# Kernel optimization log

Hardware: AMD Instinct MI355X
Metric: run time of the kernel (lower is better)

The kernel has to match this reference:

```python
import jax, jax.numpy as jnp
import numpy as np

T, EQ, N, H, K_HOPS, K_POOL = 4, 4096, 8192, 32, 2, 3


def setup_inputs() -> dict:
    key = jax.random.key(0)
    ks = jax.random.split(key, 6)
    s = 1.0 / np.sqrt(H)
    return {
        "edge_index": jax.random.randint(ks[0], (T, 2, EQ), 0, N),
        "W_gcn": jax.random.normal(ks[1], (1, H), jnp.float32) * 0.5,
        "b_gcn": jnp.zeros((H,), jnp.float32),
        "W_ih": jax.random.normal(ks[2], (3 * H, H), jnp.float32) * s,
        "W_hh": jax.random.normal(ks[3], (3 * H, H), jnp.float32) * s,
        "b_ih": jax.random.normal(ks[4], (3 * H,), jnp.float32) * s,
        "b_hh": jax.random.normal(ks[5], (3 * H,), jnp.float32) * s,
        "num_nodes": N,
    }


def _reach(seeds, src, dst, num_nodes, k):
    # k-hop reachability masks, PyG k_hop_subgraph flow='source_to_target'
    # (walk edges backwards: add sources of edges whose target is reached).
    eq = seeds.shape[0]
    R = jnp.zeros((eq, num_nodes), bool).at[jnp.arange(eq), seeds].set(True)
    for _ in range(k):
        R = R.at[:, src].max(R[:, dst])
    return R


def reference(edge_index, W_gcn, b_gcn, W_ih, W_hh, b_ih, b_hh, num_nodes):
    uq = edge_index[-1, 0]  # [EQ] query-edge sources (last snapshot)
    vq = edge_index[-1, 1]  # [EQ] query-edge targets

    def per_graph(ei):
        src, dst = ei[0], ei[1]
        Ru = _reach(uq, src, dst, num_nodes, K_HOPS)  # [EQ, N]
        Rv = _reach(vq, src, dst, num_nodes, K_HOPS)
        # union of the two k-hop subgraph edge sets (dedup via OR)
        incl = (Ru[:, src] & Ru[:, dst]) | (Rv[:, src] & Rv[:, dst])  # [EQ, Eg]
        # per-node in-degree within the merged subgraph (degree of edge_index[1])
        deg = jnp.zeros((uq.shape[0], num_nodes), jnp.float32)
        deg = deg.at[:, dst].add(incl.astype(jnp.float32))
        # global_sort_pool(k=3): top-3 nodes by the (single) degree feature,
        # zero-padded if the subgraph has <3 positive-degree nodes
        return jax.lax.top_k(deg, K_POOL)[0]  # [EQ, 3]

    tops = jax.vmap(per_graph)(edge_index)  # [T, EQ, 3]

    # GCNConv(1, H) on the 3 pooled nodes (self-loop-normalized: x @ W + b), ReLU
    h = jax.nn.relu(tops[..., None] * W_gcn[0] + b_gcn)  # [T, EQ, 3, H]

    # GRU over T snapshots, batch = EQ*3 pooled nodes
    x_seq = h.reshape(h.shape[0], -1, H)  # [T, EQ*3, H]
    h0 = jnp.zeros((x_seq.shape[1], H), x_seq.dtype)

    def cell(hprev, x):
        gi = x @ W_ih.T + b_ih
        gh = hprev @ W_hh.T + b_hh
        ir, iz, ig = jnp.split(gi, 3, axis=-1)
        hr, hz, hg = jnp.split(gh, 3, axis=-1)
        r = jax.nn.sigmoid(ir + hr)
        z = jax.nn.sigmoid(iz + hz)
        n = jnp.tanh(ig + r * hg)
        hnew = (1.0 - z) * n + z * hprev
        return hnew, None

    hn, _ = jax.lax.scan(cell, h0, x_seq)
    # stacked hidden_list: one [3, H] state per query edge
    return hn.reshape(-1, K_POOL, H)  # [EQ, 3, H]
```

## Files before the change

kernel.cpp:

```cpp
#include <hip/hip_runtime.h>
#include <hip/hip_bf16.h>
#include <math.h>

#define T_SNAP 4
#define EQn 4096
#define Nn 8192
#define Hn 32
#define NWn (Nn/32)
#define CAP 256

typedef __attribute__((ext_vector_type(4))) float f32x4;
typedef __attribute__((ext_vector_type(8))) short s16x8;

__global__ __launch_bounds__(512) void csr_build(const int* __restrict__ ei,
                                                 unsigned* __restrict__ rp,
                                                 unsigned* __restrict__ csr) {
  __shared__ unsigned cnt[Nn];
  __shared__ unsigned part[512];
  const int t = blockIdx.x;
  const int tid = threadIdx.x;
  const int* src = ei + t * 2 * EQn;
  const int* dst = src + EQn;

  for (int i = tid; i < Nn; i += 512) cnt[i] = 0u;
  __syncthreads();
  for (int e = tid; e < EQn; e += 512) atomicAdd(&cnt[dst[e]], 1u);
  __syncthreads();

  unsigned loc[16];
  unsigned s = 0u;
  const int base = tid * 16;
#pragma unroll
  for (int i = 0; i < 16; i++) { loc[i] = s; s += cnt[base + i]; }
  part[tid] = s;
  __syncthreads();
  for (int off = 1; off < 512; off <<= 1) {
    unsigned v = (tid >= off) ? part[tid - off] : 0u;
    __syncthreads();
    part[tid] += v;
    __syncthreads();
  }
  const unsigned excl = (tid == 0) ? 0u : part[tid - 1];
#pragma unroll
  for (int i = 0; i < 16; i++) {
    unsigned v = excl + loc[i];
    rp[t * (Nn + 1) + base + i] = v;
    cnt[base + i] = v;
  }
  if (tid == 0) rp[t * (Nn + 1) + Nn] = EQn;
  __syncthreads();

  for (int e = tid; e < EQn; e += 512) {
    int d = dst[e];
    unsigned slot = atomicAdd(&cnt[d], 1u);
    csr[t * EQn + slot] = (unsigned)src[e];
  }
}

__global__ __launch_bounds__(256) void reach_topk(const int* __restrict__ ei,
                                                  const unsigned* __restrict__ rp,
                                                  const unsigned* __restrict__ csr,
                                                  float* __restrict__ tops) {
  __shared__ unsigned bitsU[4][NWn];
  __shared__ unsigned bitsV[4][NWn];
  __shared__ unsigned short listU[4][CAP];
  __shared__ unsigned short listV[4][CAP];
  __shared__ unsigned cnts[4][2];

  const int w = threadIdx.x >> 6;
  const int lane = threadIdx.x & 63;
  const int gw = blockIdx.x * 4 + w;
  const int t = gw >> 12;
  const int q = gw & (EQn - 1);

  unsigned* bu = bitsU[w];
  unsigned* bv = bitsV[w];
  unsigned short* lu = listU[w];
  unsigned short* lv = listV[w];

  for (int i = lane; i < NWn; i += 64) { bu[i] = 0u; bv[i] = 0u; }
  __syncthreads();
  if (lane == 0) {
    const unsigned u = (unsigned)ei[(T_SNAP - 1) * 2 * EQn + q];
    const unsigned v = (unsigned)ei[(T_SNAP - 1) * 2 * EQn + EQn + q];
    atomicOr(&bu[u >> 5], 1u << (u & 31));
    atomicOr(&bv[v >> 5], 1u << (v & 31));
    lu[0] = (unsigned short)u;
    lv[0] = (unsigned short)v;
    cnts[w][0] = 1u;
    cnts[w][1] = 1u;
  }
  __syncthreads();

  const unsigned* rpt = rp + t * (Nn + 1);
  const unsigned* ct = csr + t * EQn;

  unsigned fsU = 0u, fsV = 0u;
  for (int hop = 0; hop < 2; hop++) {
    unsigned feU = cnts[w][0]; if (feU > CAP) feU = CAP;
    unsigned feV = cnts[w][1]; if (feV > CAP) feV = CAP;
    for (unsigned i = fsU + lane; i < feU; i += 64) {
      const unsigned n = lu[i];
      const unsigned b0 = rpt[n], b1 = rpt[n + 1];
      for (unsigned idx = b0; idx < b1; idx++) {
        const unsigned sN = ct[idx];
        const unsigned m = 1u << (sN & 31);
        const unsigned old = atomicOr(&bu[sN >> 5], m);
        if (!(old & m)) {
          unsigned pos = atomicAdd(&cnts[w][0], 1u);
          if (pos < CAP) lu[pos] = (unsigned short)sN;
        }
      }
    }
    for (unsigned i = fsV + lane; i < feV; i += 64) {
      const unsigned n = lv[i];
      const unsigned b0 = rpt[n], b1 = rpt[n + 1];
      for (unsigned idx = b0; idx < b1; idx++) {
        const unsigned sN = ct[idx];
        const unsigned m = 1u << (sN & 31);
        const unsigned old = atomicOr(&bv[sN >> 5], m);
        if (!(old & m)) {
          unsigned pos = atomicAdd(&cnts[w][1], 1u);
          if (pos < CAP) lv[pos] = (unsigned short)sN;
        }
      }
    }
    fsU = feU;
    fsV = feV;
    __syncthreads();
  }

  const unsigned cu = min(cnts[w][0], (unsigned)CAP);
  const unsigned cv = min(cnts[w][1], (unsigned)CAP);
  int a0 = 0, a1 = 0, a2 = 0;

  for (unsigned i = lane; i < cu; i += 64) {
    const unsigned n = lu[i];
    const bool nv = (bv[n >> 5] >> (n & 31)) & 1u;
    const unsigned b0 = rpt[n], b1 = rpt[n + 1];
    int d = 0;
    for (unsigned idx = b0; idx < b1; idx++) {
      const unsigned sN = ct[idx];
      const bool su = (bu[sN >> 5] >> (sN & 31)) & 1u;
      const bool sv = (bv[sN >> 5] >> (sN & 31)) & 1u;
      d += (su || (nv && sv)) ? 1 : 0;
    }
    a2 = max(a2, min(a1, d)); a1 = max(a1, min(a0, d)); a0 = max(a0, d);
  }
  for (unsigned i = lane; i < cv; i += 64) {
    const unsigned n = lv[i];
    if ((bu[n >> 5] >> (n & 31)) & 1u) continue;
    const unsigned b0 = rpt[n], b1 = rpt[n + 1];
    int d = 0;
    for (unsigned idx = b0; idx < b1; idx++) {
      const unsigned sN = ct[idx];
      d += (bv[sN >> 5] >> (sN & 31)) & 1u;
    }
    a2 = max(a2, min(a1, d)); a1 = max(a1, min(a0, d)); a0 = max(a0, d);
  }

#pragma unroll
  for (int m = 1; m < 64; m <<= 1) {
    const int b0 = __shfl_xor(a0, m);
    const int b1 = __shfl_xor(a1, m);
    const int b2 = __shfl_xor(a2, m);
    const int r0 = max(a0, b0);
    const int r1 = max(min(a0, b0), max(a1, b1));
    const int r2 = max(max(a2, b2), max(min(a1, b0), min(a0, b1)));
    a0 = r0; a1 = r1; a2 = r2;
  }
  if (lane == 0) {
    float* o = tops + (size_t)(t * EQn + q) * 3;
    o[0] = (float)a0;
    o[1] = (float)a1;
    o[2] = (float)a2;
  }
}

__device__ __forceinline__ short f2bfs(float x) {
  __hip_bfloat16 h = __float2bfloat16(x);
  short s;
  __builtin_memcpy(&s, &h, 2);
  return s;
}

__global__ __launch_bounds__(256) void gru_kernel(
    const float* __restrict__ tops,
    const float* __restrict__ Wg, const float* __restrict__ bg,
    const float* __restrict__ Wih, const float* __restrict__ Whh,
    const float* __restrict__ bih, const float* __restrict__ bhh,
    float* __restrict__ out) {
  __shared__ short hbuf[4][16 * Hn];
  const int w = threadIdx.x >> 6;
  const int lane = threadIdx.x & 63;
  const int quad = lane >> 4;
  const int c = lane & 15;
  const int waveg = blockIdx.x * 4 + w;
  const int rowbase = waveg * 16;

  s16x8 Bih[6], Bhh[6];
#pragma unroll
  for (int g = 0; g < 6; g++) {
    const int row = g * 16 + c;
#pragma unroll
    for (int j = 0; j < 8; j++) {
      Bih[g][j] = f2bfs(Wih[row * Hn + quad * 8 + j]);
      Bhh[g][j] = f2bfs(Whh[row * Hn + quad * 8 + j]);
    }
  }
  float wgv[8], bgv[8];
#pragma unroll
  for (int j = 0; j < 8; j++) {
    wgv[j] = Wg[quad * 8 + j];
    bgv[j] = bg[quad * 8 + j];
  }
  float bihv[6], bhhv[6];
#pragma unroll
  for (int g = 0; g < 6; g++) {
    bihv[g] = bih[g * 16 + c];
    bhhv[g] = bhh[g * 16 + c];
  }

  f32x4 hc0 = {0.f, 0.f, 0.f, 0.f};
  f32x4 hc1 = {0.f, 0.f, 0.f, 0.f};
  s16x8 hfrag = {0, 0, 0, 0, 0, 0, 0, 0};
  const f32x4 z4 = {0.f, 0.f, 0.f, 0.f};

  for (int t = 0; t < T_SNAP; t++) {
    const float top = tops[t * (EQn * 3) + rowbase + c];
    s16x8 xf;
#pragma unroll
    for (int j = 0; j < 8; j++) {
      float x = top * wgv[j] + bgv[j];
      x = x > 0.f ? x : 0.f;
      xf[j] = f2bfs(x);
    }
    f32x4 gi[6], gh[6];
#pragma unroll
    for (int g = 0; g < 6; g++) {
      gi[g] = __builtin_amdgcn_mfma_f32_16x16x32_bf16(xf, Bih[g], z4, 0, 0, 0);
      gh[g] = __builtin_amdgcn_mfma_f32_16x16x32_bf16(hfrag, Bhh[g], z4, 0, 0, 0);
    }
#pragma unroll
    for (int r = 0; r < 4; r++) {
      float rA = 1.f / (1.f + expf(-(gi[0][r] + bihv[0] + gh[0][r] + bhhv[0])));
      float zA = 1.f / (1.f + expf(-(gi[2][r] + bihv[2] + gh[2][r] + bhhv[2])));
      float nA = tanhf(gi[4][r] + bihv[4] + rA * (gh[4][r] + bhhv[4]));
      hc0[r] = (1.f - zA) * nA + zA * hc0[r];
      float rB = 1.f / (1.f + expf(-(gi[1][r] + bihv[1] + gh[1][r] + bhhv[1])));
      float zB = 1.f / (1.f + expf(-(gi[3][r] + bihv[3] + gh[3][r] + bhhv[3])));
      float nB = tanhf(gi[5][r] + bihv[5] + rB * (gh[5][r] + bhhv[5]));
      hc1[r] = (1.f - zB) * nB + zB * hc1[r];
    }
    if (t < T_SNAP - 1) {
      __syncthreads();
#pragma unroll
      for (int r = 0; r < 4; r++) {
        const int row = quad * 4 + r;
        hbuf[w][row * Hn + c] = f2bfs(hc0[r]);
        hbuf[w][row * Hn + 16 + c] = f2bfs(hc1[r]);
      }
      __syncthreads();
      hfrag = *reinterpret_cast<const s16x8*>(&hbuf[w][c * Hn + quad * 8]);
    }
  }
#pragma unroll
  for (int r = 0; r < 4; r++) {
    const int grow = rowbase + quad * 4 + r;
    out[grow * Hn + c] = hc0[r];
    out[grow * Hn + 16 + c] = hc1[r];
  }
}

extern "C" void kernel_launch(void* const* d_in, const int* in_sizes, int n_in,
                              void* d_out, int out_size, void* d_ws, size_t ws_size,
                              hipStream_t stream) {
  const int* ei = (const int*)d_in[0];
  const float* Wg = (const float*)d_in[1];
  const float* bg = (const float*)d_in[2];
  const float* Wih = (const float*)d_in[3];
  const float* Whh = (const float*)d_in[4];
  const float* bih = (const float*)d_in[5];
  const float* bhh = (const float*)d_in[6];

  unsigned char* ws = (unsigned char*)d_ws;
  unsigned* rp = (unsigned*)ws;
  unsigned* csr = (unsigned*)(ws + (size_t)T_SNAP * (Nn + 1) * 4);
  float* tops = (float*)(ws + (size_t)T_SNAP * (Nn + 1) * 4
                            + (size_t)T_SNAP * EQn * 4);

  csr_build<<<T_SNAP, 512, 0, stream>>>(ei, rp, csr);
  reach_topk<<<(T_SNAP * EQn) / 4, 256, 0, stream>>>(ei, rp, csr, tops);
  gru_kernel<<<(EQn * 3) / 64, 256, 0, stream>>>(tops, Wg, bg, Wih, Whh, bih, bhh,
                                                 (float*)d_out);
}
```

Measured before the change: 104.7 us.

## Split U/V reach across half-waves, use wave-shuffle scan, fast GRU math

The reach kernel now gives each half-wavefront one of the two seeds (u or v), so both BFS expansions and both degree passes run concurrently instead of back to back. The first hop expands the seed's CSR row in parallel, and blocks shrink to two wavefronts. The CSR build's prefix sum switches from a shared-memory Hillis-Steele scan with many barriers to a wave-level shuffle scan. The GRU kernel uses vectorized weight loads and fast exp/rcp-based sigmoid and tanh, trading a little accuracy for fewer instructions.

```diff
diff --git a/kernel.cpp b/kernel.cpp
--- a/kernel.cpp
+++ b/kernel.cpp
@@ -16,9 +16,11 @@
                                                  unsigned* __restrict__ rp,
                                                  unsigned* __restrict__ csr) {
   __shared__ unsigned cnt[Nn];
-  __shared__ unsigned part[512];
+  __shared__ unsigned wpart[8];
   const int t = blockIdx.x;
   const int tid = threadIdx.x;
+  const int lane = tid & 63;
+  const int wv = tid >> 6;
   const int* src = ei + t * 2 * EQn;
   const int* dst = src + EQn;
 
@@ -32,15 +34,20 @@
   const int base = tid * 16;
 #pragma unroll
   for (int i = 0; i < 16; i++) { loc[i] = s; s += cnt[base + i]; }
-  part[tid] = s;
-  __syncthreads();
-  for (int off = 1; off < 512; off <<= 1) {
-    unsigned v = (tid >= off) ? part[tid - off] : 0u;
-    __syncthreads();
-    part[tid] += v;
-    __syncthreads();
-  }
-  const unsigned excl = (tid == 0) ? 0u : part[tid - 1];
+  unsigned x = s;
+#pragma unroll
+  for (int off = 1; off < 64; off <<= 1) {
+    unsigned y = __shfl_up(x, off);
+    if (lane >= off) x += y;
+  }
+  if (lane == 63) wpart[wv] = x;
+  __syncthreads();
+  if (tid == 0) {
+    unsigned a = 0u;
+    for (int i = 0; i < 8; i++) { unsigned v = wpart[i]; wpart[i] = a; a += v; }
+  }
+  __syncthreads();
+  const unsigned excl = wpart[wv] + (x - s);
 #pragma unroll
   for (int i = 0; i < 16; i++) {
     unsigned v = excl + loc[i];
@@ -57,104 +64,89 @@
   }
 }
 
-__global__ __launch_bounds__(256) void reach_topk(const int* __restrict__ ei,
+__global__ __launch_bounds__(128) void reach_topk(const int* __restrict__ ei,
                                                   const unsigned* __restrict__ rp,
                                                   const unsigned* __restrict__ csr,
                                                   float* __restrict__ tops) {
-  __shared__ unsigned bitsU[4][NWn];
-  __shared__ unsigned bitsV[4][NWn];
-  __shared__ unsigned short listU[4][CAP];
-  __shared__ unsigned short listV[4][CAP];
-  __shared__ unsigned cnts[4][2];
+  __shared__ unsigned bits[2][2][NWn];
+  __shared__ unsigned short lists[2][2][CAP];
+  __shared__ unsigned cnts[2][2];
 
   const int w = threadIdx.x >> 6;
   const int lane = threadIdx.x & 63;
-  const int gw = blockIdx.x * 4 + w;
+  const int h = lane >> 5;
+  const int l = lane & 31;
+  const int gw = blockIdx.x * 2 + w;
   const int t = gw >> 12;
   const int q = gw & (EQn - 1);
 
-  unsigned* bu = bitsU[w];
-  unsigned* bv = bitsV[w];
-  unsigned short* lu = listU[w];
-  unsigned short* lv = listV[w];
-
-  for (int i = lane; i < NWn; i += 64) { bu[i] = 0u; bv[i] = 0u; }
-  __syncthreads();
-  if (lane == 0) {
-    const unsigned u = (unsigned)ei[(T_SNAP - 1) * 2 * EQn + q];
-    const unsigned v = (unsigned)ei[(T_SNAP - 1) * 2 * EQn + EQn + q];
-    atomicOr(&bu[u >> 5], 1u << (u & 31));
-    atomicOr(&bv[v >> 5], 1u << (v & 31));
-    lu[0] = (unsigned short)u;
-    lv[0] = (unsigned short)v;
-    cnts[w][0] = 1u;
-    cnts[w][1] = 1u;
+  unsigned* bset = bits[w][h];
+  unsigned short* lst = lists[w][h];
+
+  for (int i = l; i < NWn; i += 32) bset[i] = 0u;
+  const unsigned seed = (unsigned)ei[(T_SNAP - 1) * 2 * EQn + h * EQn + q];
+  __syncthreads();
+  if (l == 0) {
+    bset[seed >> 5] = 1u << (seed & 31);
+    lst[0] = (unsigned short)seed;
+    cnts[w][h] = 1u;
   }
   __syncthreads();
 
   const unsigned* rpt = rp + t * (Nn + 1);
   const unsigned* ct = csr + t * EQn;
 
-  unsigned fsU = 0u, fsV = 0u;
-  for (int hop = 0; hop < 2; hop++) {
-    unsigned feU = cnts[w][0]; if (feU > CAP) feU = CAP;
-    unsigned feV = cnts[w][1]; if (feV > CAP) feV = CAP;
-    for (unsigned i = fsU + lane; i < feU; i += 64) {
-      const unsigned n = lu[i];
+  {
+    const unsigned b0 = rpt[seed], b1 = rpt[seed + 1];
+    for (unsigned idx = b0 + l; idx < b1; idx += 32) {
+      const unsigned sN = ct[idx];
+      const unsigned m = 1u << (sN & 31);
+      const unsigned old = atomicOr(&bset[sN >> 5], m);
+      if (!(old & m)) {
+        unsigned pos = atomicAdd(&cnts[w][h], 1u);
+        if (pos < CAP) lst[pos] = (unsigned short)sN;
+      }
+    }
+  }
+  __syncthreads();
+
+  {
+    const unsigned fe = min(cnts[w][h], (unsigned)CAP);
+    for (unsigned i = 1 + l; i < fe; i += 32) {
+      const unsigned n = lst[i];
       const unsigned b0 = rpt[n], b1 = rpt[n + 1];
       for (unsigned idx = b0; idx < b1; idx++) {
         const unsigned sN = ct[idx];
         const unsigned m = 1u << (sN & 31);
-        const unsigned old = atomicOr(&bu[sN >> 5], m);
+        const unsigned old = atomicOr(&bset[sN >> 5], m);
         if (!(old & m)) {
-          unsigned pos = atomicAdd(&cnts[w][0], 1u);
-          if (pos < CAP) lu[pos] = (unsigned short)sN;
+          unsigned pos = atomicAdd(&cnts[w][h], 1u);
+          if (pos < CAP) lst[pos] = (unsigned short)sN;
         }
       }
     }
-    for (unsigned i = fsV + lane; i < feV; i += 64) {
-      const unsigned n = lv[i];
-      const unsigned b0 = rpt[n], b1 = rpt[n + 1];
-      for (unsigned idx = b0; idx < b1; idx++) {
-        const unsigned sN = ct[idx];
-        const unsigned m = 1u << (sN & 31);
-        const unsigned old = atomicOr(&bv[sN >> 5], m);
-        if (!(old & m)) {
-          unsigned pos = atomicAdd(&cnts[w][1], 1u);
-          if (pos < CAP) lv[pos] = (unsigned short)sN;
-        }
-      }
-    }
-    fsU = feU;
-    fsV = feV;
-    __syncthreads();
-  }
-
-  const unsigned cu = min(cnts[w][0], (unsigned)CAP);
-  const unsigned cv = min(cnts[w][1], (unsigned)CAP);
+  }
+  __syncthreads();
+
+  const unsigned* bu = bits[w][0];
+  const unsigned* bv = bits[w][1];
+  const unsigned cn = min(cnts[w][h], (unsigned)CAP);
   int a0 = 0, a1 = 0, a2 = 0;
-
-  for (unsigned i = lane; i < cu; i += 64) {
-    const unsigned n = lu[i];
+  for (unsigned i = l; i < cn; i += 32) {
+    const unsigned n = lst[i];
+    if (h == 1 && ((bu[n >> 5] >> (n & 31)) & 1u)) continue;
     const bool nv = (bv[n >> 5] >> (n & 31)) & 1u;
     const unsigned b0 = rpt[n], b1 = rpt[n + 1];
     int d = 0;
     for (unsigned idx = b0; idx < b1; idx++) {
       const unsigned sN = ct[idx];
-      const bool su = (bu[sN >> 5] >> (sN & 31)) & 1u;
-      const bool sv = (bv[sN >> 5] >> (sN & 31)) & 1u;
-      d += (su || (nv && sv)) ? 1 : 0;
-    }
-    a2 = max(a2, min(a1, d)); a1 = max(a1, min(a0, d)); a0 = max(a0, d);
-  }
-  for (unsigned i = lane; i < cv; i += 64) {
-    const unsigned n = lv[i];
-    if ((bu[n >> 5] >> (n & 31)) & 1u) continue;
-    const unsigned b0 = rpt[n], b1 = rpt[n + 1];
-    int d = 0;
-    for (unsigned idx = b0; idx < b1; idx++) {
-      const unsigned sN = ct[idx];
-      d += (bv[sN >> 5] >> (sN & 31)) & 1u;
+      if (h == 0) {
+        const bool su = (bu[sN >> 5] >> (sN & 31)) & 1u;
+        const bool sv = (bv[sN >> 5] >> (sN & 31)) & 1u;
+        d += (su || (nv && sv)) ? 1 : 0;
+      } else {
+        d += (bv[sN >> 5] >> (sN & 31)) & 1u;
+      }
     }
     a2 = max(a2, min(a1, d)); a1 = max(a1, min(a0, d)); a0 = max(a0, d);
   }
@@ -182,6 +174,12 @@
   short s;
   __builtin_memcpy(&s, &h, 2);
   return s;
+}
+__device__ __forceinline__ float sigm(float x) {
+  return __builtin_amdgcn_rcpf(1.f + __expf(-x));
+}
+__device__ __forceinline__ float tanhfast(float x) {
+  return 1.f - 2.f * __builtin_amdgcn_rcpf(1.f + __expf(2.f * x));
 }
 
 __global__ __launch_bounds__(256) void gru_kernel(
@@ -198,21 +196,32 @@
   const int waveg = blockIdx.x * 4 + w;
   const int rowbase = waveg * 16;
 
+  const f32x4* Wih4 = reinterpret_cast<const f32x4*>(Wih);
+  const f32x4* Whh4 = reinterpret_cast<const f32x4*>(Whh);
   s16x8 Bih[6], Bhh[6];
 #pragma unroll
   for (int g = 0; g < 6; g++) {
     const int row = g * 16 + c;
-#pragma unroll
-    for (int j = 0; j < 8; j++) {
-      Bih[g][j] = f2bfs(Wih[row * Hn + quad * 8 + j]);
-      Bhh[g][j] = f2bfs(Whh[row * Hn + quad * 8 + j]);
-    }
-  }
+    const int v4 = row * (Hn / 4) + quad * 2;
+    f32x4 wa = Wih4[v4], wb = Wih4[v4 + 1];
+    f32x4 ha = Whh4[v4], hb = Whh4[v4 + 1];
+#pragma unroll
+    for (int j = 0; j < 4; j++) {
+      Bih[g][j] = f2bfs(wa[j]);
+      Bih[g][j + 4] = f2bfs(wb[j]);
+      Bhh[g][j] = f2bfs(ha[j]);
+      Bhh[g][j + 4] = f2bfs(hb[j]);
+    }
+  }
+  const f32x4* Wg4 = reinterpret_cast<const f32x4*>(Wg);
+  const f32x4* bg4 = reinterpret_cast<const f32x4*>(bg);
+  f32x4 wga = Wg4[quad * 2], wgb = Wg4[quad * 2 + 1];
+  f32x4 bga = bg4[quad * 2], bgb = bg4[quad * 2 + 1];
   float wgv[8], bgv[8];
 #pragma unroll
-  for (int j = 0; j < 8; j++) {
-    wgv[j] = Wg[quad * 8 + j];
-    bgv[j] = bg[quad * 8 + j];
+  for (int j = 0; j < 4; j++) {
+    wgv[j] = wga[j]; wgv[j + 4] = wgb[j];
+    bgv[j] = bga[j]; bgv[j + 4] = bgb[j];
   }
   float bihv[6], bhhv[6];
 #pragma unroll
@@ -243,13 +252,13 @@
     }
 #pragma unroll
     for (int r = 0; r < 4; r++) {
-      float rA = 1.f / (1.f + expf(-(gi[0][r] + bihv[0] + gh[0][r] + bhhv[0])));
-      float zA = 1.f / (1.f + expf(-(gi[2][r] + bihv[2] + gh[2][r] + bhhv[2])));
-      float nA = tanhf(gi[4][r] + bihv[4] + rA * (gh[4][r] + bhhv[4]));
+      float rA = sigm(gi[0][r] + bihv[0] + gh[0][r] + bhhv[0]);
+      float zA = sigm(gi[2][r] + bihv[2] + gh[2][r] + bhhv[2]);
+      float nA = tanhfast(gi[4][r] + bihv[4] + rA * (gh[4][r] + bhhv[4]));
       hc0[r] = (1.f - zA) * nA + zA * hc0[r];
-      float rB = 1.f / (1.f + expf(-(gi[1][r] + bihv[1] + gh[1][r] + bhhv[1])));
-      float zB = 1.f / (1.f + expf(-(gi[3][r] + bihv[3] + gh[3][r] + bhhv[3])));
-      float nB = tanhf(gi[5][r] + bihv[5] + rB * (gh[5][r] + bhhv[5]));
+      float rB = sigm(gi[1][r] + bihv[1] + gh[1][r] + bhhv[1]);
+      float zB = sigm(gi[3][r] + bihv[3] + gh[3][r] + bhhv[3]);
+      float nB = tanhfast(gi[5][r] + bihv[5] + rB * (gh[5][r] + bhhv[5]));
       hc1[r] = (1.f - zB) * nB + zB * hc1[r];
     }
     if (t < T_SNAP - 1) {
@@ -290,7 +299,7 @@
                             + (size_t)T_SNAP * EQn * 4);
 
   csr_build<<<T_SNAP, 512, 0, stream>>>(ei, rp, csr);
-  reach_topk<<<(T_SNAP * EQn) / 4, 256, 0, stream>>>(ei, rp, csr, tops);
+  reach_topk<<<(T_SNAP * EQn) / 2, 128, 0, stream>>>(ei, rp, csr, tops);
   gru_kernel<<<(EQn * 3) / 64, 256, 0, stream>>>(tops, Wg, bg, Wih, Whh, bih, bhh,
                                                  (float*)d_out);
 }
```

After: 93.35 us. 10.8% less time.
